# Kernel optimization log

Measured on AMD Instinct MI355X. Metric: run time of the kernel, lower is better.

## Reference

```python
import jax, jax.numpy as jnp
import numpy as np

EPS = 1e-12  # torch F.normalize eps


def unfold(x, ksize, pad):
    # torch F.unfold equivalent: [B,C,H,W] -> [B, C*k*k, L], channel-major ordering
    patches = jax.lax.conv_general_dilated_patches(
        x, (ksize, ksize), (1, 1), [(pad, pad), (pad, pad)],
        dimension_numbers=('NCHW', 'OIHW', 'NCHW'))
    B, CKK, Hp, Wp = patches.shape
    return patches.reshape(B, CKK, Hp * Wp)


def fold(patches, C, ksize, H, W, pad):
    # torch F.fold equivalent (stride 1): overlap-add of [B, C*k*k, H*W] -> [B,C,H,W]
    B = patches.shape[0]
    p = patches.reshape(B, C, ksize, ksize, H, W)
    out = jnp.zeros((B, C, H + 2 * pad, W + 2 * pad), patches.dtype)
    for di in range(ksize):
        for dj in range(ksize):
            out = out.at[:, :, di:di + H, dj:dj + W].add(p[:, :, di, dj])
    return out[:, :, pad:pad + H, pad:pad + W]


def setup_inputs() -> dict:
    key = jax.random.key(0)
    ks = jax.random.split(key, 4)
    B, C, H, W = 2, 512, 64, 64
    D, CIN = 256, 512 * 9  # embed: Linear(tdim*8*3*3 -> tdim*4), tdim=64
    return {
        'query': jax.random.normal(ks[0], (B, C, H, W), dtype=jnp.float32),
        'key': jax.random.normal(ks[1], (B, C, H, W), dtype=jnp.float32),
        'value': jax.random.normal(ks[2], (B, C, H, W), dtype=jnp.float32),
        'W_embed': jax.random.normal(ks[3], (D, CIN), dtype=jnp.float32) * 0.02,
        'k': 3,
    }


def reference(query, key, value, W_embed, k):
    B, Cv, H, W = value.shape
    # patch embed: unfold -> linear (no bias)
    q_unf = unfold(query, k, k // 2)                       # [B, C*k*k, L]
    k_unf = unfold(key, k, k // 2)                         # [B, C*k*k, L]
    k_emb = jnp.einsum('bcl,dc->bld', k_unf, W_embed)      # [B, L, D]
    q_emb = jnp.einsum('bcl,dc->bdl', q_unf, W_embed)      # [B, D, L]
    # cosine correlation
    k_n = k_emb / jnp.maximum(jnp.linalg.norm(k_emb, axis=2, keepdims=True), EPS)
    q_n = q_emb / jnp.maximum(jnp.linalg.norm(q_emb, axis=1, keepdims=True), EPS)
    corr = jnp.einsum('bld,bdm->blm', k_n, q_n)            # [B, L_key, L_query]
    corr_value = jnp.max(corr, axis=1)                     # [B, L]
    corr_argmax = jnp.argmax(corr, axis=1)                 # [B, L]
    # swap(V=value, idx=corr_argmax, s=1, k=k)
    s = 1
    temph = s * k + H * s - H - s                          # = k - 1
    tempw = s * k + W * s - W - s
    ph = max(temph // 2 + temph % 2, 1)
    pw = max(tempw // 2 + tempw % 2, 1)
    v_unf = unfold(value, k, ph)                           # [B, Cv*k*k, L] (ph==pw for square)
    t_unf = jnp.take_along_axis(v_unf, corr_argmax[:, None, :], axis=2)
    divisor = fold(jnp.ones_like(t_unf), Cv, k, H, W, ph)
    T = fold(t_unf, Cv, k, H, W, ph) / divisor             # [B, Cv, H, W]
    S = corr_value.reshape(B, 1, H, W)
    return S, T
```

## Files before the change

kernel.cpp:

```cpp
#include <hip/hip_runtime.h>
#include <hip/hip_bf16.h>
#include <stdint.h>
#include <math.h>

#define BB 2
#define CC 512
#define HH 64
#define WW 64
#define LL 4096
#define DD 256
#define CIN 4608
#define NG 144

typedef _Float16 half_t;
typedef __attribute__((ext_vector_type(8))) _Float16 f16x8;
typedef __attribute__((ext_vector_type(4))) _Float16 f16x4;
typedef __attribute__((ext_vector_type(4))) float f32x4;

__global__ __launch_bounds__(256) void presplit(const float* __restrict__ query,
                                                const float* __restrict__ key,
                                                char* __restrict__ img_ts) {
    __shared__ float tile[32][65];
    int img = blockIdx.y;
    int y   = blockIdx.x;
    const float* src = ((img >> 1) ? key : query) + (size_t)(img & 1) * CC * LL + y * WW;
    char* dstbase = img_ts + ((size_t)img * 64 + y) * (16 * 64 * 128);
    int t = threadIdx.x;
    int xl = t & 63, c4 = t >> 6;
    int xw = t >> 2, fsw = t & 3;
    for (int cc = 0; cc < 16; ++cc) {
#pragma unroll
        for (int j = 0; j < 8; ++j) {
            int cl = c4 + j * 4;
            tile[cl][xl] = src[(size_t)(cc * 32 + cl) * LL + xl];
        }
        __syncthreads();
        f16x8 h8, l8;
#pragma unroll
        for (int j = 0; j < 8; ++j) {
            float v = tile[fsw * 8 + j][xw];
            half_t h = (half_t)v;
            h8[j] = h; l8[j] = (half_t)(v - (float)h);
        }
        char* p = dstbase + (size_t)cc * 8192 + xw * 128;
        int swz = (xw & 7) << 4;
        *(f16x8*)(p + ((fsw * 16) ^ swz)) = h8;
        *(f16x8*)(p + ((64 + fsw * 16) ^ swz)) = l8;
        __syncthreads();
    }
}

__global__ __launch_bounds__(256) void splitW2b(const float* __restrict__ W,
                                                char* __restrict__ Wst) {
    int i = blockIdx.x * 256 + threadIdx.x;
    if (i >= NG * DD * 4) return;
    int g  = i >> 10;
    int r  = i & 1023;
    int d  = r >> 2;
    int fs = r & 3;
    int cc = g / 9, o = g - cc * 9;
    const float* src = W + (size_t)d * CIN;
    f16x8 h8, l8;
#pragma unroll
    for (int j = 0; j < 8; j++) {
        float w = src[(cc * 32 + fs * 8 + j) * 9 + o];
        half_t h = (half_t)w;
        h8[j] = h;
        l8[j] = (half_t)(w - (float)h);
    }
    size_t base = (size_t)g * 32768 + d * 128;
    int sw = (d & 7) << 4;
    *(f16x8*)(Wst + base + ((fs * 16) ^ sw)) = h8;
    *(f16x8*)(Wst + base + ((64 + fs * 16) ^ sw)) = l8;
}

#define GATE() do { asm volatile("s_waitcnt vmcnt(0) lgkmcnt(0)" ::: "memory"); \
                    __builtin_amdgcn_s_barrier(); \
                    __builtin_amdgcn_sched_barrier(0); } while (0)

__global__ __launch_bounds__(512, 2) void embed_mfma(const char* __restrict__ img_ts,
                                                     const char* __restrict__ Wst,
                                                     const char* __restrict__ zp,
                                                     float* __restrict__ part) {
    __shared__ char sW[2][32768];
    __shared__ char sB[2][33792];

    int iid = blockIdx.y;
    int ks  = blockIdx.z;
    int lt  = blockIdx.x;
    int y0  = lt * 2;
    int t = threadIdx.x;
    int w = t >> 6, lane = t & 63;
    int wr = w >> 1, wc = w & 1;
    int fr = lane & 15, fs = lane >> 4;

    const char* imgb = img_ts + (size_t)iid * (64 * 16 * 64 * 128) + (size_t)ks * 65536;
    const char *ps0, *ps1, *ps2, *ps3, *ps4;
    int pb0, pb1, pb2, pb3, pb4;
#define PREP(qv, PS, PB)                                                \
    {                                                                   \
        int q = (qv);                                                   \
        int ri = q / 528;                                               \
        int rem = q - ri * 528;                                         \
        int xi = rem >> 3, sub = rem & 7;                               \
        int xg = xi - 1, yg = y0 - 1 + ri;                              \
        bool ok = (yg >= 0) && (yg < 64) && (xg >= 0) && (xg < 64);     \
        PS = ok ? imgb + (size_t)yg * 131072 + (size_t)xg * 128 + sub * 16 \
                : zp + ((q & 255) * 16);                                \
        PB = ok ? 8192 : 0;                                             \
    }
    PREP(t, ps0, pb0); PREP(512 + t, ps1, pb1); PREP(1024 + t, ps2, pb2);
    PREP(1536 + t, ps3, pb3); PREP(2048 + t, ps4, pb4);

    const char* pW = Wst + (size_t)ks * 72 * 32768;

#define GLL(src, dst)                                                   \
    __builtin_amdgcn_global_load_lds(                                   \
        (const __attribute__((address_space(1))) void*)(src),           \
        (__attribute__((address_space(3))) void*)(dst), 16, 0, 0)

#define DMAW(dst)                                                       \
    do {                                                                \
        _Pragma("unroll")                                               \
        for (int c = 0; c < 4; c++)                                     \
            GLL(pW + c * 8192 + t * 16, (dst) + c * 8192 + t * 16);     \
        pW += 32768;                                                    \
    } while (0)

#define DMAB(dst)                                                       \
    do {                                                                \
        GLL(ps0, (dst) + t * 16);                                       \
        GLL(ps1, (dst) + 8192 + t * 16);                                \
        GLL(ps2, (dst) + 16384 + t * 16);                               \
        GLL(ps3, (dst) + 24576 + t * 16);                               \
        if (t < 64) GLL(ps4, (dst) + 32768 + t * 16);                   \
        ps0 += pb0; ps1 += pb1; ps2 += pb2; ps3 += pb3; ps4 += pb4;     \
    } while (0)

#define READA(AH, AL, wbuf)                                             \
    do {                                                                \
        _Pragma("unroll")                                               \
        for (int rg = 0; rg < 4; rg++) {                                \
            int dl = wr * 64 + rg * 16 + fr;                            \
            int sw_ = (dl & 7) << 4;                                    \
            const char* rowp = (const char*)(wbuf) + dl * 128;          \
            AH[rg] = *(const f16x8*)(rowp + ((fs * 16) ^ sw_));         \
            AL[rg] = *(const f16x8*)(rowp + ((64 + fs * 16) ^ sw_));    \
        }                                                               \
    } while (0)

#define READB(BH, BL, bbuf, di_, dj_)                                   \
    do {                                                                \
        int ri = wc + (di_);                                            \
        _Pragma("unroll")                                               \
        for (int cg = 0; cg < 4; cg++) {                                \
            int xi = cg * 16 + fr + (dj_);                              \
            int sw_ = ((xi - 1) & 7) << 4;                              \
            const char* rowp = (const char*)(bbuf) + ri * 8448 + xi * 128; \
            BH[cg] = *(const f16x8*)(rowp + ((fs * 16) ^ sw_));         \
            BL[cg] = *(const f16x8*)(rowp + ((64 + fs * 16) ^ sw_));    \
        }                                                               \
    } while (0)

#define DOMFMA(AH, AL, BH, BL)                                          \
    do {                                                                \
        _Pragma("unroll")                                               \
        for (int rg = 0; rg < 4; rg++)                                  \
            _Pragma("unroll")                                           \
            for (int cg = 0; cg < 4; cg++)                              \
                acc[rg][cg] = __builtin_amdgcn_mfma_f32_16x16x32_f16(AH[rg], BH[cg], acc[rg][cg], 0, 0, 0); \
        _Pragma("unroll")                                               \
        for (int rg = 0; rg < 4; rg++)                                  \
            _Pragma("unroll")                                           \
            for (int cg = 0; cg < 4; cg++) {                            \
                acc[rg][cg] = __builtin_amdgcn_mfma_f32_16x16x32_f16(AH[rg], BL[cg], acc[rg][cg], 0, 0, 0); \
                acc[rg][cg] = __builtin_amdgcn_mfma_f32_16x16x32_f16(AL[rg], BH[cg], acc[rg][cg], 0, 0, 0); \
            }                                                           \
    } while (0)

    f32x4 acc[4][4];
#pragma unroll
    for (int rg = 0; rg < 4; rg++)
#pragma unroll
        for (int cg = 0; cg < 4; cg++) acc[rg][cg] = (f32x4){0.f, 0.f, 0.f, 0.f};

    f16x8 ah0[4], al0[4], bh0[4], bl0[4];
    f16x8 ah1[4], al1[4], bh1[4], bl1[4];

    char* wb0 = &sW[0][0]; char* wb1 = &sW[1][0];
    char* b0 = &sB[0][0];  char* b1 = &sB[1][0];

    DMAB(b0);
    DMAW(wb0);
    GATE();
    READA(ah0, al0, wb0);
    READB(bh0, bl0, b0, 0, 0);
    DMAW(wb1);
    GATE();

#pragma unroll 1
    for (int g = 0; g < 72; g += 2) {
        {
            int g1 = g + 1;
            int c1 = g1 / 9, o1 = g1 - c1 * 9;
            int di_ = (o1 >= 6) ? 2 : (o1 >= 3) ? 1 : 0;
            int dj_ = o1 - di_ * 3;
            READA(ah1, al1, wb1);
            READB(bh1, bl1, (c1 & 1) ? b1 : b0, di_, dj_);
        }
        if (g + 2 < 72) DMAW(wb0);
        {
            int cg_ = g / 9;
            int c2 = cg_ + 1;
            if (g - cg_ * 9 == 7 && c2 < 8) DMAB((c2 & 1) ? b1 : b0);
        }
        __builtin_amdgcn_sched_barrier(0);
        DOMFMA(ah0, al0, bh0, bl0);
        GATE();
        if (g + 2 < 72) {
            int g2 = g + 2;
            int c1 = g2 / 9, o1 = g2 - c1 * 9;
            int di_ = (o1 >= 6) ? 2 : (o1 >= 3) ? 1 : 0;
            int dj_ = o1 - di_ * 3;
            READA(ah0, al0, wb0);
            READB(bh0, bl0, (c1 & 1) ? b1 : b0, di_, dj_);
            if (g + 3 < 72) DMAW(wb1);
            int g1v = g + 1;
            int cg_ = g1v / 9;
            int c2 = cg_ + 1;
            if (g1v - cg_ * 9 == 7 && c2 < 8) DMAB((c2 & 1) ? b1 : b0);
        }
        __builtin_amdgcn_sched_barrier(0);
        DOMFMA(ah1, al1, bh1, bl1);
        GATE();
    }

    float* pt = part + (((size_t)iid * 32 + lt) * 2 + ks) * 32768;
#pragma unroll
    for (int rg = 0; rg < 4; rg++)
#pragma unroll
        for (int cg = 0; cg < 4; cg++) {
            int l = wc * 64 + cg * 16 + fr;
            int d0 = wr * 64 + rg * 16 + fs * 4;
#pragma unroll
            for (int r = 0; r < 4; r++)
                pt[(d0 + r) * 128 + l] = acc[rg][cg][r];
        }
#undef PREP
#undef GLL
#undef DMAW
#undef DMAB
#undef READA
#undef READB
#undef DOMFMA
}

__global__ __launch_bounds__(256) void norm_split(const float* __restrict__ part,
                                                  char* __restrict__ qemb,
                                                  char* __restrict__ kemb) {
    __shared__ float sm[4][64];
    __shared__ float invn[64];
    __shared__ char stage[64][1040];

    int iid = blockIdx.y;
    int bx  = blockIdx.x;
    int lt  = bx >> 1, lh2 = bx & 1;
    const float* p0 = part + (((size_t)iid * 32 + lt) * 2 + 0) * 32768 + lh2 * 64;
    const float* p1 = p0 + 32768;
    int t = threadIdx.x;
    int ll = t & 63, dq = t >> 6;

    float sq = 0.f;
    for (int dd = 0; dd < 64; ++dd) {
        int d = dq * 64 + dd;
        float v = p0[d * 128 + ll] + p1[d * 128 + ll];
        sq += v * v;
    }
    sm[dq][ll] = sq;
    __syncthreads();
    if (t < 64) {
        float s = sm[0][t] + sm[1][t] + sm[2][t] + sm[3][t];
        invn[t] = 1.0f / fmaxf(sqrtf(s), 1e-12f);
    }
    __syncthreads();

    float sc = invn[ll];
    int swb = (ll & 7) << 4;
    for (int oc = 0; oc < 8; ++oc) {
        int d0 = dq * 64 + oc * 8;
        f16x8 h8, l8;
#pragma unroll
        for (int j = 0; j < 8; ++j) {
            int d = d0 + j;
            float v = (p0[d * 128 + ll] + p1[d * 128 + ll]) * sc;
            half_t h = (half_t)v;
            h8[j] = h;
            l8[j] = (half_t)(v - (float)h);
        }
        int itb = d0 >> 5;
        int fsc = (d0 >> 3) & 3;
        *(f16x8*)&stage[ll][itb * 128 + ((fsc * 16) ^ swb)] = h8;
        *(f16x8*)&stage[ll][itb * 128 + ((64 + fsc * 16) ^ swb)] = l8;
    }
    __syncthreads();

    int b = iid & 1, type = iid >> 1;
    char* e = (type ? kemb : qemb);
    int rr = t >> 2, c0 = t & 3;
    char* erow = e + ((size_t)b * LL + lt * 128 + lh2 * 64 + rr) * 1024;
    const char* srow = &stage[rr][0];
#pragma unroll
    for (int c = 0; c < 16; ++c) {
        int cj = c0 + c * 4;
        *(float4*)(erow + cj * 16) = *(const float4*)(srow + cj * 16);
    }
}

__global__ void init_packed(unsigned long long* p, int n) {
    int i = blockIdx.x * 256 + threadIdx.x;
    if (i < n) p[i] = 0ull;
}

__global__ __launch_bounds__(256, 2) void corr_max_mfma(const char* __restrict__ kemb,
                                                        const char* __restrict__ qemb,
                                                        unsigned long long* __restrict__ packed) {
    __shared__ char sA[2][16384];
    __shared__ char sBq[2][16384];

    int b  = blockIdx.z;
    int l0 = blockIdx.y * 128;
    int m0 = blockIdx.x * 128;
    int t  = threadIdx.x;
    int w = t >> 6, lane = t & 63;
    int wr = w >> 1, wc = w & 1;
    int fr = lane & 15, fs = lane >> 4;

    const char* Abase = kemb + ((size_t)b * LL + l0) * 1024;
    const char* Bbase = qemb + ((size_t)b * LL + m0) * 1024;

    f32x4 acc[4][4];
#pragma unroll
    for (int i = 0; i < 4; i++)
#pragma unroll
        for (int j = 0; j < 4; j++) acc[i][j] = (f32x4){0.f, 0.f, 0.f, 0.f};

#define DMA2(bufi, itv)                                                   \
    do {                                                                  \
        _Pragma("unroll")                                                 \
        for (int c = 0; c < 4; c++) {                                     \
            int idx = c * 4096 + t * 16;                                  \
            int row = idx >> 7, offb = idx & 127;                         \
            __builtin_amdgcn_global_load_lds(                             \
                (const __attribute__((address_space(1))) void*)(Abase + (size_t)row * 1024 + (itv) * 128 + offb), \
                (__attribute__((address_space(3))) void*)(&sA[bufi][idx]), 16, 0, 0); \
        }                                                                 \
        _Pragma("unroll")                                                 \
        for (int c = 0; c < 4; c++) {                                     \
            int idx = c * 4096 + t * 16;                                  \
            int row = idx >> 7, offb = idx & 127;                         \
            __builtin_amdgcn_global_load_lds(                             \
                (const __attribute__((address_space(1))) void*)(Bbase + (size_t)row * 1024 + (itv) * 128 + offb), \
                (__attribute__((address_space(3))) void*)(&sBq[bufi][idx]), 16, 0, 0); \
        }                                                                 \
    } while (0)

    DMA2(0, 0);

    f16x8 ah[4], al[4], bh[4], bl[4];
    for (int it = 0; it < 8; ++it) {
        asm volatile("s_waitcnt vmcnt(0) lgkmcnt(0)" ::: "memory");
        __builtin_amdgcn_s_barrier();
        __builtin_amdgcn_sched_barrier(0);
        if (it < 7) DMA2((it + 1) & 1, it + 1);
        __builtin_amdgcn_sched_barrier(0);
        const char* sa = sA[it & 1];
        const char* sb = sBq[it & 1];
#pragma unroll
        for (int rg = 0; rg < 4; rg++) {
            int r = wr * 64 + rg * 16 + fr;
            const char* rp = sa + r * 128;
            int sw_ = (r & 7) << 4;
            ah[rg] = *(const f16x8*)(rp + ((fs * 16) ^ sw_));
            al[rg] = *(const f16x8*)(rp + ((64 + fs * 16) ^ sw_));
        }
#pragma unroll
        for (int cg = 0; cg < 4; cg++) {
            int r = wc * 64 + cg * 16 + fr;
            const char* rp = sb + r * 128;
            int sw_ = (r & 7) << 4;
            bh[cg] = *(const f16x8*)(rp + ((fs * 16) ^ sw_));
            bl[cg] = *(const f16x8*)(rp + ((64 + fs * 16) ^ sw_));
        }
#pragma unroll
        for (int rg = 0; rg < 4; rg++)
#pragma unroll
            for (int cg = 0; cg < 4; cg++)
                acc[rg][cg] = __builtin_amdgcn_mfma_f32_16x16x32_f16(ah[rg], bh[cg], acc[rg][cg], 0, 0, 0);
#pragma unroll
        for (int rg = 0; rg < 4; rg++)
#pragma unroll
            for (int cg = 0; cg < 4; cg++) {
                acc[rg][cg] = __builtin_amdgcn_mfma_f32_16x16x32_f16(ah[rg], bl[cg], acc[rg][cg], 0, 0, 0);
                acc[rg][cg] = __builtin_amdgcn_mfma_f32_16x16x32_f16(al[rg], bh[cg], acc[rg][cg], 0, 0, 0);
            }
    }
#undef DMA2

#pragma unroll
    for (int cg = 0; cg < 4; cg++) {
        unsigned long long best = 0ull;
#pragma unroll
        for (int rg = 0; rg < 4; rg++) {
#pragma unroll
            for (int r = 0; r < 4; r++) {
                unsigned u = __float_as_uint(acc[rg][cg][r]);
                u = (u & 0x80000000u) ? ~u : (u | 0x80000000u);
                int l = l0 + wr * 64 + rg * 16 + fs * 4 + r;
                unsigned long long p = ((unsigned long long)u << 32) | (unsigned)(4095 - l);
                best = (p > best) ? p : best;
            }
        }
        unsigned long long oo;
        oo = __shfl_xor(best, 16); best = (oo > best) ? oo : best;
        oo = __shfl_xor(best, 32); best = (oo > best) ? oo : best;
        if (lane < 16)
            atomicMax(&packed[(size_t)b * LL + m0 + wc * 64 + cg * 16 + lane], best);
    }
}

__global__ void decode_packed(const unsigned long long* __restrict__ packed,
                              float* __restrict__ S_out, int* __restrict__ arg) {
    int i = blockIdx.x * 256 + threadIdx.x;
    if (i < BB * LL) {
        unsigned long long p = packed[i];
        unsigned u = (unsigned)(p >> 32);
        unsigned bits = (u & 0x80000000u) ? (u & 0x7FFFFFFFu) : ~u;
        S_out[i] = __uint_as_float(bits);
        arg[i] = 4095 - (int)(unsigned)(p & 0xFFFFFFFFull);
    }
}

__global__ __launch_bounds__(256) void transpose_mat(const float* __restrict__ src,
                                                     float* __restrict__ dst,
                                                     int R, int Cc) {
    __shared__ float tile[32][33];
    size_t boff = (size_t)blockIdx.z * R * Cc;
    int bx = blockIdx.x;
    int by = blockIdx.y;
    int tx = threadIdx.x & 31;
    int ty = threadIdx.x >> 5;
    const float* s = src + boff;
    float* d = dst + boff;
#pragma unroll
    for (int i = 0; i < 4; i++) {
        int r = by * 32 + ty + i * 8;
        int c = bx * 32 + tx;
        tile[ty + i * 8][tx] = s[(size_t)r * Cc + c];
    }
    __syncthreads();
#pragma unroll
    for (int i = 0; i < 4; i++) {
        int c = bx * 32 + ty + i * 8;
        int r = by * 32 + tx;
        d[(size_t)c * R + r] = tile[tx][ty + i * 8];
    }
}

__global__ __launch_bounds__(256) void gather_fold(const float* __restrict__ value_t,
                                                   const int* __restrict__ arg,
                                                   float* __restrict__ T_t) {
    int b = blockIdx.y;
    int pix = blockIdx.x;
    int y = pix >> 6, x = pix & 63;
    int t = threadIdx.x;
    float2 acc = make_float2(0.f, 0.f);
    int cnty = (y == 0 || y == HH - 1) ? 2 : 3;
    int cntx = (x == 0 || x == WW - 1) ? 2 : 3;
    const int* ab = arg + b * LL;
    const float* vb = value_t + (size_t)b * LL * CC;
#pragma unroll
    for (int di = 0; di < 3; di++) {
        int my = y + 1 - di;
        if (my < 0 || my >= HH) continue;
#pragma unroll
        for (int dj = 0; dj < 3; dj++) {
            int mx = x + 1 - dj;
            if (mx < 0 || mx >= WW) continue;
            int a = ab[my * WW + mx];
            int ay = a >> 6, ax = a & 63;
            int vy = ay + di - 1, vx = ax + dj - 1;
            if (vy < 0 || vy >= HH || vx < 0 || vx >= WW) continue;
            float2 v = *(const float2*)&vb[((size_t)(vy * WW + vx)) * CC + t * 2];
            acc.x += v.x; acc.y += v.y;
        }
    }
    float inv = 1.0f / (float)(cnty * cntx);
    acc.x *= inv; acc.y *= inv;
    *(float2*)&T_t[((size_t)b * LL + pix) * CC + t * 2] = acc;
}

extern "C" void kernel_launch(void* const* d_in, const int* in_sizes, int n_in,
                              void* d_out, int out_size, void* d_ws, size_t ws_size,
                              hipStream_t stream) {
    const float* query = (const float*)d_in[0];
    const float* key   = (const float*)d_in[1];
    const float* value = (const float*)d_in[2];
    const float* Wemb  = (const float*)d_in[3];

    float* out   = (float*)d_out;
    float* S_out = out;
    float* T_out = out + BB * LL;

    char* ws = (char*)d_ws;
    char*  img_ts = ws;
    char*  Wst    = ws + 33554432;
    float* part   = (float*)(ws + 38273024);
    char*  qemb   = ws + 71827456;
    char*  kemb   = ws + 80216064;
    unsigned long long* packed = (unsigned long long*)(ws + 88604672);
    char*  zp     = ws + 88670208;
    int*   arg    = (int*)(ws + 88674304);
    float* val_t  = (float*)(ws + 38273024);
    float* T_t    = (float*)(ws + 38273024 + 16777216);

    init_packed   <<<dim3(34), 256, 0, stream>>>(packed, 8704);
    presplit      <<<dim3(64, 4), 256, 0, stream>>>(query, key, img_ts);
    splitW2b      <<<dim3(576), 256, 0, stream>>>(Wemb, Wst);
    embed_mfma    <<<dim3(32, 4, 2), 512, 0, stream>>>(img_ts, Wst, zp, part);
    norm_split    <<<dim3(64, 4), 256, 0, stream>>>(part, qemb, kemb);
    corr_max_mfma <<<dim3(32, 32, 2), 256, 0, stream>>>(kemb, qemb, packed);
    decode_packed <<<dim3(32), 256, 0, stream>>>(packed, S_out, arg);
    transpose_mat <<<dim3(128, 16, 2), 256, 0, stream>>>(value, val_t, CC, LL);
    gather_fold   <<<dim3(4096, 2), 256, 0, stream>>>(val_t, arg, T_t);
    transpose_mat <<<dim3(16, 128, 2), 256, 0, stream>>>(T_t, T_out, LL, CC);
}
```

Measured before the change: 219.0 us.

## Read embed weights directly from global memory and prefetch image tiles earlier

The weight tiles are no longer staged through LDS with global_load_lds. Each wave now loads its A fragments straight from global memory into registers, which frees 64KB of shared memory. The image-tile DMA is issued earlier in each channel group (offset 1 instead of 7), and barriers wait only on LDS counters except at the group boundary, where a partial vmcnt(8) wait is used. Launch bounds drop to 1 block per SM, which adds register room. The risk is that direct global weight reads carry more latency, and the vmcnt accounting may not match the actual outstanding loads.

```diff
diff --git a/kernel.cpp b/kernel.cpp
--- a/kernel.cpp
+++ b/kernel.cpp
@@ -74,15 +74,20 @@
     *(f16x8*)(Wst + base + ((64 + fs * 16) ^ sw)) = l8;
 }
 
-#define GATE() do { asm volatile("s_waitcnt vmcnt(0) lgkmcnt(0)" ::: "memory"); \
-                    __builtin_amdgcn_s_barrier(); \
-                    __builtin_amdgcn_sched_barrier(0); } while (0)
-
-__global__ __launch_bounds__(512, 2) void embed_mfma(const char* __restrict__ img_ts,
+#define GATE_L()  do { asm volatile("s_waitcnt lgkmcnt(0)" ::: "memory"); \
+                       __builtin_amdgcn_s_barrier(); \
+                       __builtin_amdgcn_sched_barrier(0); } while (0)
+#define GATE_V8() do { asm volatile("s_waitcnt vmcnt(8) lgkmcnt(0)" ::: "memory"); \
+                       __builtin_amdgcn_s_barrier(); \
+                       __builtin_amdgcn_sched_barrier(0); } while (0)
+#define GATE0()   do { asm volatile("s_waitcnt vmcnt(0) lgkmcnt(0)" ::: "memory"); \
+                       __builtin_amdgcn_s_barrier(); \
+                       __builtin_amdgcn_sched_barrier(0); } while (0)
+
+__global__ __launch_bounds__(512, 1) void embed_mfma(const char* __restrict__ img_ts,
                                                      const char* __restrict__ Wst,
                                                      const char* __restrict__ zp,
                                                      float* __restrict__ part) {
-    __shared__ char sW[2][32768];
     __shared__ char sB[2][33792];
 
     int iid = blockIdx.y;
@@ -112,20 +117,12 @@
     PREP(t, ps0, pb0); PREP(512 + t, ps1, pb1); PREP(1024 + t, ps2, pb2);
     PREP(1536 + t, ps3, pb3); PREP(2048 + t, ps4, pb4);
 
-    const char* pW = Wst + (size_t)ks * 72 * 32768;
+    const char* Wks = Wst + (size_t)ks * 72 * 32768;
 
 #define GLL(src, dst)                                                   \
     __builtin_amdgcn_global_load_lds(                                   \
         (const __attribute__((address_space(1))) void*)(src),           \
         (__attribute__((address_space(3))) void*)(dst), 16, 0, 0)
-
-#define DMAW(dst)                                                       \
-    do {                                                                \
-        _Pragma("unroll")                                               \
-        for (int c = 0; c < 4; c++)                                     \
-            GLL(pW + c * 8192 + t * 16, (dst) + c * 8192 + t * 16);     \
-        pW += 32768;                                                    \
-    } while (0)
 
 #define DMAB(dst)                                                       \
     do {                                                                \
@@ -137,13 +134,14 @@
         ps0 += pb0; ps1 += pb1; ps2 += pb2; ps3 += pb3; ps4 += pb4;     \
     } while (0)
 
-#define READA(AH, AL, wbuf)                                             \
+#define READAG(AH, AL, gv)                                              \
     do {                                                                \
+        const char* wg_ = Wks + (size_t)(gv) * 32768;                   \
         _Pragma("unroll")                                               \
         for (int rg = 0; rg < 4; rg++) {                                \
             int dl = wr * 64 + rg * 16 + fr;                            \
             int sw_ = (dl & 7) << 4;                                    \
-            const char* rowp = (const char*)(wbuf) + dl * 128;          \
+            const char* rowp = wg_ + dl * 128;                          \
             AH[rg] = *(const f16x8*)(rowp + ((fs * 16) ^ sw_));         \
             AL[rg] = *(const f16x8*)(rowp + ((64 + fs * 16) ^ sw_));    \
         }                                                               \
@@ -187,16 +185,14 @@
     f16x8 ah0[4], al0[4], bh0[4], bl0[4];
     f16x8 ah1[4], al1[4], bh1[4], bl1[4];
 
-    char* wb0 = &sW[0][0]; char* wb1 = &sW[1][0];
-    char* b0 = &sB[0][0];  char* b1 = &sB[1][0];
+    char* b0 = &sB[0][0];
+    char* b1 = &sB[1][0];
 
     DMAB(b0);
-    DMAW(wb0);
-    GATE();
-    READA(ah0, al0, wb0);
+    READAG(ah0, al0, 0);
+    GATE0();
     READB(bh0, bl0, b0, 0, 0);
-    DMAW(wb1);
-    GATE();
+    __builtin_amdgcn_sched_barrier(0);
 
 #pragma unroll 1
     for (int g = 0; g < 72; g += 2) {
@@ -205,34 +201,30 @@
             int c1 = g1 / 9, o1 = g1 - c1 * 9;
             int di_ = (o1 >= 6) ? 2 : (o1 >= 3) ? 1 : 0;
             int dj_ = o1 - di_ * 3;
-            READA(ah1, al1, wb1);
+            READAG(ah1, al1, g1);
             READB(bh1, bl1, (c1 & 1) ? b1 : b0, di_, dj_);
         }
-        if (g + 2 < 72) DMAW(wb0);
         {
             int cg_ = g / 9;
-            int c2 = cg_ + 1;
-            if (g - cg_ * 9 == 7 && c2 < 8) DMAB((c2 & 1) ? b1 : b0);
+            if (g - cg_ * 9 == 1 && cg_ < 7) DMAB(((cg_ + 1) & 1) ? b1 : b0);
         }
         __builtin_amdgcn_sched_barrier(0);
         DOMFMA(ah0, al0, bh0, bl0);
-        GATE();
+        if (g % 9 == 7) GATE_V8(); else GATE_L();
         if (g + 2 < 72) {
             int g2 = g + 2;
             int c1 = g2 / 9, o1 = g2 - c1 * 9;
             int di_ = (o1 >= 6) ? 2 : (o1 >= 3) ? 1 : 0;
             int dj_ = o1 - di_ * 3;
-            READA(ah0, al0, wb0);
+            READAG(ah0, al0, g2);
             READB(bh0, bl0, (c1 & 1) ? b1 : b0, di_, dj_);
-            if (g + 3 < 72) DMAW(wb1);
             int g1v = g + 1;
             int cg_ = g1v / 9;
-            int c2 = cg_ + 1;
-            if (g1v - cg_ * 9 == 7 && c2 < 8) DMAB((c2 & 1) ? b1 : b0);
+            if (g1v - cg_ * 9 == 1 && cg_ < 7) DMAB(((cg_ + 1) & 1) ? b1 : b0);
         }
         __builtin_amdgcn_sched_barrier(0);
         DOMFMA(ah1, al1, bh1, bl1);
-        GATE();
+        if ((g + 1) % 9 == 7) GATE_V8(); else GATE_L();
     }
 
     float* pt = part + (((size_t)iid * 32 + lt) * 2 + ks) * 32768;
@@ -248,9 +240,8 @@
         }
 #undef PREP
 #undef GLL
-#undef DMAW
 #undef DMAB
-#undef READA
+#undef READAG
 #undef READB
 #undef DOMFMA
 }
```

Result: slower. 249.4 us (+13.9%).
